# Performance work log

Measured on AMD Instinct MI355X. Metric: run time of the kernel, lower is better.

Reference implementation:

```python
import jax, jax.numpy as jnp
import numpy as np

B, P, Q, N, D, K_HEADCHUNK = 16, 12, 12, 2048, 64, 8


def setup_inputs() -> dict:
    key = jax.random.key(0)
    ks = jax.random.split(key, 8)
    mkw = lambda k, sh: (jax.random.normal(k, sh, jnp.float32) * 0.05)
    return {
        "x": jax.random.normal(ks[0], (B, P, N, D), jnp.float32),
        "STE_P": jax.random.normal(ks[1], (B, P, N, D), jnp.float32),
        "STE_Q": jax.random.normal(ks[2], (B, Q, N, D), jnp.float32),
        # shared input projection (applied to query, key AND value in the original)
        "W_ff": mkw(ks[3], (D, D)), "b_ff": jnp.zeros((D,), jnp.float32),
        # two-layer output FFN
        "W1": mkw(ks[4], (D, D)), "b1": jnp.zeros((D,), jnp.float32),
        "W2": mkw(ks[5], (D, D)), "b2": jnp.zeros((D,), jnp.float32),
        "K": K_HEADCHUNK,
    }


def reference(x, STE_P, STE_Q, W_ff, b_ff, W1, b1, W2, b2, K):
    # Faithful to torch source: split(..., K, dim=-1) makes chunks of SIZE K,
    # i.e. h = D // K heads (h == self.d), each with head_dim K. Scale is d**0.5.
    Dm = x.shape[-1]
    h = Dm // K                      # number of heads (= self.d in torch code)
    scale = 1.0 / np.sqrt(float(h))  # attention /= self.d ** 0.5

    q = STE_Q @ W_ff + b_ff          # [B, Q, N, D]
    k = STE_P @ W_ff + b_ff          # [B, P, N, D]
    v = x @ W_ff + b_ff              # [B, P, N, D]

    Bb, Tq, Nn = q.shape[0], q.shape[1], q.shape[2]
    Tp = k.shape[1]
    qh = q.reshape(Bb, Tq, Nn, h, K)
    kh = k.reshape(Bb, Tp, Nn, h, K)
    vh = v.reshape(Bb, Tp, Nn, h, K)

    scores = jnp.einsum('bqnhk,bpnhk->bhnqp', qh, kh) * scale  # [B,h,N,Q,P]
    attn = jax.nn.softmax(scores, axis=-1)
    out = jnp.einsum('bhnqp,bpnhk->bqnhk', attn, vh).reshape(Bb, Tq, Nn, Dm)

    hid = jax.nn.relu(out @ W1 + b1)
    return hid @ W2 + b2             # [B, Q, N, D]
```

## Files before the change

kernel.cpp:

```cpp
#include <hip/hip_runtime.h>
#include <hip/hip_bf16.h>


typedef __attribute__((ext_vector_type(8))) short bf16x8;
typedef __attribute__((ext_vector_type(4))) float f32x4;

constexpr int Bb = 16, Ss = 12, Nn = 2048, Dd = 64;
constexpr float EXPK = 0.51011687f;
constexpr int KOFS = 12288, VOFS = 24576, LDSZ = 36864;

#define MFMA16(A, B, C) __builtin_amdgcn_mfma_f32_16x16x32_bf16((A), (B), (C), 0, 0, 0)

__device__ __forceinline__ short f2bf(float f) {
    __hip_bfloat16 h = __float2bfloat16(f);
    short s; __builtin_memcpy(&s, &h, 2); return s;
}
__device__ __forceinline__ float bitf(unsigned u) {
    float f; __builtin_memcpy(&f, &u, 4); return f;
}
__device__ __forceinline__ float bf2f(unsigned short v) {
    return bitf(((unsigned)v) << 16);
}
__device__ __forceinline__ unsigned cvtpk(float lo, float hi) {
    unsigned r;
    asm("v_cvt_pk_bf16_f32 %0, %1, %2" : "=v"(r) : "v"(lo), "v"(hi));
    return r;
}
__device__ __forceinline__ void lds_fence() {
    asm volatile("s_waitcnt lgkmcnt(0)" ::: "memory");
    __builtin_amdgcn_sched_barrier(0);
}
__device__ __forceinline__ int qkOfs(int t, int s, int n, int d) {
    return t * KOFS + s * 1024 + n * 128 + ((2 * d) ^ (((s & 7) ^ (n & 7)) << 4));
}
__device__ __forceinline__ int tOfs(int w, int row, int d) {
    return w * 3072 + row * 128 + ((2 * d) ^ ((row & 7) << 4));
}

__global__ void prep_w(const float* __restrict__ Wff, const float* __restrict__ W1,
                       const float* __restrict__ W2, unsigned short* __restrict__ wt) {
    int idx = blockIdx.x * 256 + threadIdx.x;
    if (idx >= 3 * 4096) return;
    int m = idx >> 12, rc = idx & 4095, r = rc >> 6, c = rc & 63;
    const float* W = (m == 0) ? Wff : (m == 1) ? W1 : W2;
    unsigned short u; short s = f2bf(W[c * 64 + r]);
    __builtin_memcpy(&u, &s, 2);
    wt[idx] = u;
}

__global__ __launch_bounds__(512, 4)
void ta_mfma7(const float* __restrict__ x,
              const float* __restrict__ steP,
              const float* __restrict__ steQ,
              const float* __restrict__ bff, const float* __restrict__ b1,
              const float* __restrict__ b2,
              const unsigned short* __restrict__ wt,
              float* __restrict__ out)
{
    alignas(16) __shared__ char smem[LDSZ];

    const int tid = threadIdx.x;
    const int w   = tid >> 6;
    const int l   = tid & 63;
    const int l15 = l & 15;
    const int l4  = l >> 4;
    const int b   = blockIdx.y;
    const int n0  = blockIdx.x * 8;

    bf16x8 wf[4][2];
    float bfv[4];
    #pragma unroll
    for (int nt = 0; nt < 4; ++nt) {
        bfv[nt] = bff[nt * 16 + l15];
        #pragma unroll
        for (int kc = 0; kc < 2; ++kc)
            wf[nt][kc] = *(const bf16x8*)(wt + (nt * 16 + l15) * 64 + kc * 32 + l4 * 8);
    }

    const int sA = l15 >> 3, nA = l15 & 7;
    for (int job = w; job < 18; job += 8) {
        const int t = job / 6, s0 = (job % 6) * 2;
        const float* base = (t == 0) ? steQ : (t == 1) ? steP : x;
        const float* rp = base + ((size_t)(b * Ss + s0 + sA) * Nn + n0 + nA) * Dd + l4 * 8;

        bf16x8 a[2];
        #pragma unroll
        for (int kc = 0; kc < 2; ++kc) {
            float4 p0 = *(const float4*)(rp + kc * 32);
            float4 p1 = *(const float4*)(rp + kc * 32 + 4);
            union { unsigned u[4]; bf16x8 v; } cv;
            cv.u[0] = cvtpk(p0.x, p0.y); cv.u[1] = cvtpk(p0.z, p0.w);
            cv.u[2] = cvtpk(p1.x, p1.y); cv.u[3] = cvtpk(p1.z, p1.w);
            a[kc] = cv.v;
        }
        #pragma unroll
        for (int nt = 0; nt < 4; ++nt) {
            f32x4 acc = { bfv[nt], bfv[nt], bfv[nt], bfv[nt] };
            acc = MFMA16(a[0], wf[nt][0], acc);
            acc = MFMA16(a[1], wf[nt][1], acc);
            const int d = nt * 16 + l15;
            #pragma unroll
            for (int q = 0; q < 4; ++q) {
                const int r = l4 * 4 + q, s = s0 + (r >> 3), nn = r & 7;
                *(short*)(smem + qkOfs(t, s, nn, d)) = f2bf(acc[q]);
            }
        }
    }
    __syncthreads();

    const int n = w;
    float vv[12];
    #pragma unroll
    for (int s = 0; s < 12; ++s)
        vv[s] = bf2f(*(const unsigned short*)(smem + qkOfs(2, s, n, l)));

    unsigned pw[8][2];
    #pragma unroll
    for (int h = 0; h < 8; ++h) {
        union { unsigned u[4]; bf16x8 v; } akk;
        akk.v = *(const bf16x8*)(smem + qkOfs(1, l15, n, h * 8));
        bf16x8 aq = *(const bf16x8*)(smem + qkOfs(0, l15, n, h * 8));
        if (l4 != 0) { akk.u[0] = 0; akk.u[1] = 0; akk.u[2] = 0; akk.u[3] = 0; }
        f32x4 c = { 0.f, 0.f, 0.f, 0.f };
        c = MFMA16(akk.v, aq, c);
        float e[4];
        #pragma unroll
        for (int i = 0; i < 4; ++i) {
            float v = __builtin_amdgcn_exp2f(c[i] * EXPK);
            e[i] = (l4 == 3) ? 0.f : v;
        }
        float ssum = (e[0] + e[1]) + (e[2] + e[3]);
        ssum += __shfl_xor(ssum, 16);
        ssum += __shfl_xor(ssum, 32);
        float inv;
        asm("v_rcp_f32 %0, %1" : "=v"(inv) : "v"(ssum));
        pw[h][0] = cvtpk(e[0] * inv, e[1] * inv);
        pw[h][1] = cvtpk(e[2] * inv, e[3] * inv);
    }
    __syncthreads();

    const int pb = w * 3072;
    if (l15 < 12) {
        #pragma unroll
        for (int h = 0; h < 8; ++h) {
            uint2 u; u.x = pw[h][0]; u.y = pw[h][1];
            *(uint2*)(smem + pb + l15 * 256 + ((h * 32) ^ ((l15 & 7) << 5)) + l4 * 8) = u;
        }
    }
    lds_fence();

    float oacc[12];
    const int hslot = (l >> 3) * 32;
    #pragma unroll
    for (int q = 0; q < 12; ++q) {
        const char* qp = smem + pb + q * 256 + (hslot ^ ((q & 7) << 5));
        float a = 0.f;
        #pragma unroll
        for (int p2 = 0; p2 < 6; ++p2) {
            unsigned pd = *(const unsigned*)(qp + p2 * 4);
            a = fmaf(bitf(pd << 16),         vv[2 * p2],     a);
            a = fmaf(bitf(pd & 0xFFFF0000u), vv[2 * p2 + 1], a);
        }
        oacc[q] = a;
    }
    lds_fence();

    #pragma unroll
    for (int q = 0; q < 12; ++q)
        *(short*)(smem + tOfs(w, q, l)) = f2bf(oacc[q]);
    lds_fence();

    {
        bf16x8 w1f[4][2];
        float b1v[4];
        #pragma unroll
        for (int nt = 0; nt < 4; ++nt) {
            b1v[nt] = b1[nt * 16 + l15];
            #pragma unroll
            for (int kc = 0; kc < 2; ++kc)
                w1f[nt][kc] = *(const bf16x8*)(wt + 4096 + (nt * 16 + l15) * 64 + kc * 32 + l4 * 8);
        }
        bf16x8 a[2];
        #pragma unroll
        for (int kc = 0; kc < 2; ++kc)
            a[kc] = *(const bf16x8*)(smem + tOfs(w, l15, kc * 32 + l4 * 8));
        #pragma unroll
        for (int nt = 0; nt < 4; ++nt) {
            f32x4 acc = { b1v[nt], b1v[nt], b1v[nt], b1v[nt] };
            acc = MFMA16(a[0], w1f[nt][0], acc);
            acc = MFMA16(a[1], w1f[nt][1], acc);
            #pragma unroll
            for (int reg = 0; reg < 4; ++reg) {
                const int rt = l4 * 4 + reg;
                if (rt < 12)
                    *(short*)(smem + tOfs(w, rt, nt * 16 + l15)) =
                        f2bf(fmaxf(acc[reg], 0.f));
            }
        }
    }
    lds_fence();
    {
        bf16x8 w2f[4][2];
        float b2v[4];
        #pragma unroll
        for (int nt = 0; nt < 4; ++nt) {
            b2v[nt] = b2[nt * 16 + l15];
            #pragma unroll
            for (int kc = 0; kc < 2; ++kc)
                w2f[nt][kc] = *(const bf16x8*)(wt + 8192 + (nt * 16 + l15) * 64 + kc * 32 + l4 * 8);
        }
        bf16x8 a[2];
        #pragma unroll
        for (int kc = 0; kc < 2; ++kc)
            a[kc] = *(const bf16x8*)(smem + tOfs(w, l15, kc * 32 + l4 * 8));
        #pragma unroll
        for (int nt = 0; nt < 4; ++nt) {
            f32x4 acc = { b2v[nt], b2v[nt], b2v[nt], b2v[nt] };
            acc = MFMA16(a[0], w2f[nt][0], acc);
            acc = MFMA16(a[1], w2f[nt][1], acc);
            #pragma unroll
            for (int reg = 0; reg < 4; ++reg) {
                const int q = l4 * 4 + reg;
                if (q < 12)
                    out[((size_t)(b * Ss + q) * Nn + n0 + w) * Dd + nt * 16 + l15] = acc[reg];
            }
        }
    }
}

extern "C" void kernel_launch(void* const* d_in, const int* in_sizes, int n_in,
                              void* d_out, int out_size, void* d_ws, size_t ws_size,
                              hipStream_t stream) {
    const float* x    = (const float*)d_in[0];
    const float* steP = (const float*)d_in[1];
    const float* steQ = (const float*)d_in[2];
    const float* Wff  = (const float*)d_in[3];
    const float* bff  = (const float*)d_in[4];
    const float* W1   = (const float*)d_in[5];
    const float* b1   = (const float*)d_in[6];
    const float* W2   = (const float*)d_in[7];
    const float* b2   = (const float*)d_in[8];
    float* out = (float*)d_out;
    unsigned short* wtp = (unsigned short*)d_ws;

    prep_w<<<48, 256, 0, stream>>>(Wff, W1, W2, wtp);
    dim3 grid(Nn / 8, Bb);
    ta_mfma7<<<grid, 512, 0, stream>>>(x, steP, steQ, bff, b1, b2, wtp, out);
}
```

Before: 151.1 us.

## Halve block size so each wave handles two nodes, vectorize P loads

Blocks shrink from 512 to 256 threads (4 waves), and each wave processes two spatial nodes in the attention and FFN stages. Weight fragments and bias loads are amortized over twice the work per wave. The probability reads in the PV loop become one 16-byte and one 8-byte LDS load instead of six scalar loads. The cost is fewer waves per block for latency hiding and higher register pressure from doubled per-wave arrays.

```diff
diff --git a/kernel.cpp b/kernel.cpp
--- a/kernel.cpp
+++ b/kernel.cpp
@@ -33,8 +33,8 @@
 __device__ __forceinline__ int qkOfs(int t, int s, int n, int d) {
     return t * KOFS + s * 1024 + n * 128 + ((2 * d) ^ (((s & 7) ^ (n & 7)) << 4));
 }
-__device__ __forceinline__ int tOfs(int w, int row, int d) {
-    return w * 3072 + row * 128 + ((2 * d) ^ ((row & 7) << 4));
+__device__ __forceinline__ int tOfs(int w, int ni, int row, int d) {
+    return w * 6144 + ni * 3072 + row * 128 + ((2 * d) ^ ((row & 7) << 4));
 }
 
 __global__ void prep_w(const float* __restrict__ Wff, const float* __restrict__ W1,
@@ -48,8 +48,8 @@
     wt[idx] = u;
 }
 
-__global__ __launch_bounds__(512, 4)
-void ta_mfma7(const float* __restrict__ x,
+__global__ __launch_bounds__(256, 4)
+void ta_mfma8(const float* __restrict__ x,
               const float* __restrict__ steP,
               const float* __restrict__ steQ,
               const float* __restrict__ bff, const float* __restrict__ b1,
@@ -78,7 +78,7 @@
     }
 
     const int sA = l15 >> 3, nA = l15 & 7;
-    for (int job = w; job < 18; job += 8) {
+    for (int job = w; job < 18; job += 4) {
         const int t = job / 6, s0 = (job % 6) * 2;
         const float* base = (t == 0) ? steQ : (t == 1) ? steP : x;
         const float* rp = base + ((size_t)(b * Ss + s0 + sA) * Nn + n0 + nA) * Dd + l4 * 8;
@@ -108,66 +108,81 @@
     }
     __syncthreads();
 
-    const int n = w;
-    float vv[12];
-    #pragma unroll
-    for (int s = 0; s < 12; ++s)
-        vv[s] = bf2f(*(const unsigned short*)(smem + qkOfs(2, s, n, l)));
-
-    unsigned pw[8][2];
+    float vv[2][12];
+    #pragma unroll
+    for (int ni = 0; ni < 2; ++ni)
+        #pragma unroll
+        for (int s = 0; s < 12; ++s)
+            vv[ni][s] = bf2f(*(const unsigned short*)(smem + qkOfs(2, s, w * 2 + ni, l)));
+
+    unsigned pw[2][8][2];
     #pragma unroll
     for (int h = 0; h < 8; ++h) {
-        union { unsigned u[4]; bf16x8 v; } akk;
-        akk.v = *(const bf16x8*)(smem + qkOfs(1, l15, n, h * 8));
-        bf16x8 aq = *(const bf16x8*)(smem + qkOfs(0, l15, n, h * 8));
-        if (l4 != 0) { akk.u[0] = 0; akk.u[1] = 0; akk.u[2] = 0; akk.u[3] = 0; }
-        f32x4 c = { 0.f, 0.f, 0.f, 0.f };
-        c = MFMA16(akk.v, aq, c);
-        float e[4];
-        #pragma unroll
-        for (int i = 0; i < 4; ++i) {
-            float v = __builtin_amdgcn_exp2f(c[i] * EXPK);
-            e[i] = (l4 == 3) ? 0.f : v;
-        }
-        float ssum = (e[0] + e[1]) + (e[2] + e[3]);
-        ssum += __shfl_xor(ssum, 16);
-        ssum += __shfl_xor(ssum, 32);
-        float inv;
-        asm("v_rcp_f32 %0, %1" : "=v"(inv) : "v"(ssum));
-        pw[h][0] = cvtpk(e[0] * inv, e[1] * inv);
-        pw[h][1] = cvtpk(e[2] * inv, e[3] * inv);
+        #pragma unroll
+        for (int ni = 0; ni < 2; ++ni) {
+            const int n = w * 2 + ni;
+            union { unsigned u[4]; bf16x8 v; } akk;
+            akk.v = *(const bf16x8*)(smem + qkOfs(1, l15, n, h * 8));
+            bf16x8 aq = *(const bf16x8*)(smem + qkOfs(0, l15, n, h * 8));
+            if (l4 != 0) { akk.u[0] = 0; akk.u[1] = 0; akk.u[2] = 0; akk.u[3] = 0; }
+            f32x4 c = { 0.f, 0.f, 0.f, 0.f };
+            c = MFMA16(akk.v, aq, c);
+            float e[4];
+            #pragma unroll
+            for (int i = 0; i < 4; ++i) {
+                float v = __builtin_amdgcn_exp2f(c[i] * EXPK);
+                e[i] = (l4 == 3) ? 0.f : v;
+            }
+            float ssum = (e[0] + e[1]) + (e[2] + e[3]);
+            ssum += __shfl_xor(ssum, 16);
+            ssum += __shfl_xor(ssum, 32);
+            float inv;
+            asm("v_rcp_f32 %0, %1" : "=v"(inv) : "v"(ssum));
+            pw[ni][h][0] = cvtpk(e[0] * inv, e[1] * inv);
+            pw[ni][h][1] = cvtpk(e[2] * inv, e[3] * inv);
+        }
     }
     __syncthreads();
 
-    const int pb = w * 3072;
-    if (l15 < 12) {
-        #pragma unroll
-        for (int h = 0; h < 8; ++h) {
-            uint2 u; u.x = pw[h][0]; u.y = pw[h][1];
-            *(uint2*)(smem + pb + l15 * 256 + ((h * 32) ^ ((l15 & 7) << 5)) + l4 * 8) = u;
-        }
-    }
-    lds_fence();
-
-    float oacc[12];
+    #pragma unroll
+    for (int ni = 0; ni < 2; ++ni) {
+        const int pb = w * 6144 + ni * 3072;
+        if (l15 < 12 && l4 < 3) {
+            #pragma unroll
+            for (int h = 0; h < 8; ++h) {
+                uint2 u; u.x = pw[ni][h][0]; u.y = pw[ni][h][1];
+                *(uint2*)(smem + pb + l15 * 256 + ((h * 32) ^ ((l15 & 7) << 5)) + l4 * 8) = u;
+            }
+        }
+    }
+    lds_fence();
+
+    float oacc[2][12];
     const int hslot = (l >> 3) * 32;
     #pragma unroll
     for (int q = 0; q < 12; ++q) {
-        const char* qp = smem + pb + q * 256 + (hslot ^ ((q & 7) << 5));
-        float a = 0.f;
-        #pragma unroll
-        for (int p2 = 0; p2 < 6; ++p2) {
-            unsigned pd = *(const unsigned*)(qp + p2 * 4);
-            a = fmaf(bitf(pd << 16),         vv[2 * p2],     a);
-            a = fmaf(bitf(pd & 0xFFFF0000u), vv[2 * p2 + 1], a);
-        }
-        oacc[q] = a;
-    }
-    lds_fence();
-
-    #pragma unroll
-    for (int q = 0; q < 12; ++q)
-        *(short*)(smem + tOfs(w, q, l)) = f2bf(oacc[q]);
+        #pragma unroll
+        for (int ni = 0; ni < 2; ++ni) {
+            const char* qp = smem + w * 6144 + ni * 3072 + q * 256 + (hslot ^ ((q & 7) << 5));
+            uint4 pa = *(const uint4*)(qp);
+            uint2 pbx = *(const uint2*)(qp + 16);
+            const unsigned wds[6] = { pa.x, pa.y, pa.z, pa.w, pbx.x, pbx.y };
+            float a = 0.f;
+            #pragma unroll
+            for (int p2 = 0; p2 < 6; ++p2) {
+                a = fmaf(bitf(wds[p2] << 16),         vv[ni][2 * p2],     a);
+                a = fmaf(bitf(wds[p2] & 0xFFFF0000u), vv[ni][2 * p2 + 1], a);
+            }
+            oacc[ni][q] = a;
+        }
+    }
+    lds_fence();
+
+    #pragma unroll
+    for (int ni = 0; ni < 2; ++ni)
+        #pragma unroll
+        for (int q = 0; q < 12; ++q)
+            *(short*)(smem + tOfs(w, ni, q, l)) = f2bf(oacc[ni][q]);
     lds_fence();
 
     {
@@ -180,21 +195,24 @@
             for (int kc = 0; kc < 2; ++kc)
                 w1f[nt][kc] = *(const bf16x8*)(wt + 4096 + (nt * 16 + l15) * 64 + kc * 32 + l4 * 8);
         }
-        bf16x8 a[2];
-        #pragma unroll
-        for (int kc = 0; kc < 2; ++kc)
-            a[kc] = *(const bf16x8*)(smem + tOfs(w, l15, kc * 32 + l4 * 8));
-        #pragma unroll
-        for (int nt = 0; nt < 4; ++nt) {
-            f32x4 acc = { b1v[nt], b1v[nt], b1v[nt], b1v[nt] };
-            acc = MFMA16(a[0], w1f[nt][0], acc);
-            acc = MFMA16(a[1], w1f[nt][1], acc);
-            #pragma unroll
-            for (int reg = 0; reg < 4; ++reg) {
-                const int rt = l4 * 4 + reg;
-                if (rt < 12)
-                    *(short*)(smem + tOfs(w, rt, nt * 16 + l15)) =
-                        f2bf(fmaxf(acc[reg], 0.f));
+        #pragma unroll
+        for (int ni = 0; ni < 2; ++ni) {
+            bf16x8 a[2];
+            #pragma unroll
+            for (int kc = 0; kc < 2; ++kc)
+                a[kc] = *(const bf16x8*)(smem + tOfs(w, ni, l15, kc * 32 + l4 * 8));
+            #pragma unroll
+            for (int nt = 0; nt < 4; ++nt) {
+                f32x4 acc = { b1v[nt], b1v[nt], b1v[nt], b1v[nt] };
+                acc = MFMA16(a[0], w1f[nt][0], acc);
+                acc = MFMA16(a[1], w1f[nt][1], acc);
+                #pragma unroll
+                for (int reg = 0; reg < 4; ++reg) {
+                    const int rt = l4 * 4 + reg;
+                    if (rt < 12)
+                        *(short*)(smem + tOfs(w, ni, rt, nt * 16 + l15)) =
+                            f2bf(fmaxf(acc[reg], 0.f));
+                }
             }
         }
     }
@@ -209,20 +227,23 @@
             for (int kc = 0; kc < 2; ++kc)
                 w2f[nt][kc] = *(const bf16x8*)(wt + 8192 + (nt * 16 + l15) * 64 + kc * 32 + l4 * 8);
         }
-        bf16x8 a[2];
-        #pragma unroll
-        for (int kc = 0; kc < 2; ++kc)
-            a[kc] = *(const bf16x8*)(smem + tOfs(w, l15, kc * 32 + l4 * 8));
-        #pragma unroll
-        for (int nt = 0; nt < 4; ++nt) {
-            f32x4 acc = { b2v[nt], b2v[nt], b2v[nt], b2v[nt] };
-            acc = MFMA16(a[0], w2f[nt][0], acc);
-            acc = MFMA16(a[1], w2f[nt][1], acc);
-            #pragma unroll
-            for (int reg = 0; reg < 4; ++reg) {
-                const int q = l4 * 4 + reg;
-                if (q < 12)
-                    out[((size_t)(b * Ss + q) * Nn + n0 + w) * Dd + nt * 16 + l15] = acc[reg];
+        #pragma unroll
+        for (int ni = 0; ni < 2; ++ni) {
+            bf16x8 a[2];
+            #pragma unroll
+            for (int kc = 0; kc < 2; ++kc)
+                a[kc] = *(const bf16x8*)(smem + tOfs(w, ni, l15, kc * 32 + l4 * 8));
+            #pragma unroll
+            for (int nt = 0; nt < 4; ++nt) {
+                f32x4 acc = { b2v[nt], b2v[nt], b2v[nt], b2v[nt] };
+                acc = MFMA16(a[0], w2f[nt][0], acc);
+                acc = MFMA16(a[1], w2f[nt][1], acc);
+                #pragma unroll
+                for (int reg = 0; reg < 4; ++reg) {
+                    const int q = l4 * 4 + reg;
+                    if (q < 12)
+                        out[((size_t)(b * Ss + q) * Nn + n0 + w * 2 + ni) * Dd + nt * 16 + l15] = acc[reg];
+                }
             }
         }
     }
@@ -245,5 +266,5 @@
 
     prep_w<<<48, 256, 0, stream>>>(Wff, W1, W2, wtp);
     dim3 grid(Nn / 8, Bb);
-    ta_mfma7<<<grid, 512, 0, stream>>>(x, steP, steQ, bff, b1, b2, wtp, out);
-}
+    ta_mfma8<<<grid, 256, 0, stream>>>(x, steP, steQ, bff, b1, b2, wtp, out);
+}
```

New measurement: 127.6 us. 15.5% less time.
